# Kernel tuning notes

Hardware: AMD Instinct MI355X
Metric: run time of the kernel (lower is better)

The kernel has to match this reference:

```python
import jax, jax.numpy as jnp
import numpy as np

HEADS = 16
DIM_HEAD = 64
DIM = 1024
MLP = 4096
SCALE = DIM_HEAD ** -0.5
EPS = 1e-5


def _layernorm(x, g, b):
    m = jnp.mean(x, axis=-1, keepdims=True)
    v = jnp.var(x, axis=-1, keepdims=True)
    return (x - m) * jax.lax.rsqrt(v + EPS) * g + b


def _attention(q_in, k_in, qw, kw, vw, ow, ob):
    # v = k (per module); weights stored [in, out]
    b = q_in.shape[0]
    def split(t):  # b n (h d) -> b h n d
        return t.reshape(b, t.shape[1], HEADS, DIM_HEAD).transpose(0, 2, 1, 3)
    q = split(q_in @ qw)
    k = split(k_in @ kw)
    v = split(k_in @ vw)
    dots = jnp.einsum('bhid,bhjd->bhij', q, k) * SCALE
    attn = jax.nn.softmax(dots, axis=-1)
    out = jnp.einsum('bhij,bhjd->bhid', attn, v)
    out = out.transpose(0, 2, 1, 3).reshape(b, out.shape[2], HEADS * DIM_HEAD)
    return out @ ow + ob


def setup_inputs() -> dict:
    key = jax.random.key(0)
    ks = jax.random.split(key, 24)
    def w(k, shape, fan_in):
        return jax.random.normal(k, shape, jnp.float32) * (fan_in ** -0.5)
    inner = HEADS * DIM_HEAD
    return {
        'x': jax.random.normal(ks[0], (4, 4096, DIM), jnp.float32),
        'p': jax.random.normal(ks[1], (4, 256, DIM), jnp.float32),
        'pq_w': w(ks[2], (DIM, inner), DIM), 'pk_w': w(ks[3], (DIM, inner), DIM),
        'pv_w': w(ks[4], (DIM, inner), DIM),
        'po_w': w(ks[5], (inner, DIM), inner), 'po_b': jnp.zeros((DIM,), jnp.float32),
        'xq_w': w(ks[6], (DIM, inner), DIM), 'xk_w': w(ks[7], (DIM, inner), DIM),
        'xv_w': w(ks[8], (DIM, inner), DIM),
        'xo_w': w(ks[9], (inner, DIM), inner), 'xo_b': jnp.zeros((DIM,), jnp.float32),
        'pn_g': jnp.ones((DIM,), jnp.float32), 'pn_b': jnp.zeros((DIM,), jnp.float32),
        'xn_g': jnp.ones((DIM,), jnp.float32), 'xn_b': jnp.zeros((DIM,), jnp.float32),
        'w1': w(ks[10], (DIM, MLP), DIM), 'b1': jnp.zeros((MLP,), jnp.float32),
        'w2': w(ks[11], (MLP, DIM), MLP), 'b2': jnp.zeros((DIM,), jnp.float32),
        'fn_g': jnp.ones((DIM,), jnp.float32), 'fn_b': jnp.zeros((DIM,), jnp.float32),
    }


def reference(x, p, pq_w, pk_w, pv_w, po_w, po_b, xq_w, xk_w, xv_w, xo_w, xo_b,
              pn_g, pn_b, xn_g, xn_b, w1, b1, w2, b2, fn_g, fn_b):
    # p attends to x
    p_att = _attention(p, x, pq_w, pk_w, pv_w, po_w, po_b)
    p_new = _layernorm(p_att + p, pn_g, pn_b)
    # x attends to p_att (note: keys/values come from p_att, not p_new)
    x_att = _attention(x, p_att, xq_w, xk_w, xv_w, xo_w, xo_b)
    x = _layernorm(x_att + x, xn_g, xn_b)
    x_ff = jax.nn.gelu(x @ w1 + b1, approximate=False) @ w2 + b2
    x = _layernorm(x_ff + x, fn_g, fn_b)
    return (x, p_new)
```

## Files before the change

kernel.cpp:

```cpp
#include <hip/hip_runtime.h>


typedef short bf16x8 __attribute__((ext_vector_type(8)));
typedef float f32x4 __attribute__((ext_vector_type(4)));
typedef unsigned int u32x2 __attribute__((ext_vector_type(2)));
typedef unsigned int u32x4v __attribute__((ext_vector_type(4)));

__device__ __forceinline__ unsigned cvt_pk_bf16(float a, float b) {
  unsigned r;
  asm("v_cvt_pk_bf16_f32 %0, %1, %2" : "=v"(r) : "v"(a), "v"(b));
  return r;
}
__device__ __forceinline__ bf16x8 mk8(u32x2 a, u32x2 b) {
  u32x4v t; t.x = a.x; t.y = a.y; t.z = b.x; t.w = b.y;
  return __builtin_bit_cast(bf16x8, t);
}

#define AST 36
#define SEL_LO 0x05040100u
#define SEL_HI 0x07060302u

__global__ __launch_bounds__(256, 2) void gemm_kernel(
    const float* __restrict__ A, int lda,
    const float* __restrict__ Bw, int ldb,
    const float* __restrict__ bias,
    float* __restrict__ C, int ldc,
    int K, int flags)
{
  __shared__ __align__(16) unsigned short Ah[128 * AST];
  __shared__ __align__(16) unsigned short Al[128 * AST];
  __shared__ __align__(16) unsigned short Bh[128 * AST];
  __shared__ __align__(16) unsigned short Bl[128 * AST];

  const int tid = threadIdx.x;
  const int bid   = blockIdx.y * gridDim.x + blockIdx.x;
  const int chunk = (gridDim.x * gridDim.y) >> 3;
  const int lg    = (bid & 7) * chunk + (bid >> 3);
  const int bcol  = (lg % gridDim.x) * 128;
  const int brow  = (lg / gridDim.x) * 128;

  const int lane = tid & 63;
  const int w    = tid >> 6;
  const int wr   = (w >> 1) * 64;
  const int wc   = (w & 1) * 64;
  const int ti   = lane & 15;
  const int g    = lane >> 4;

  const int arow = tid >> 3;
  const int ac4  = (tid & 7) * 4;
  const int K0   = (tid >> 5) * 4;
  const int n4   = (tid & 31) * 4;
  int bwa[4];
#pragma unroll
  for (int i = 0; i < 4; i++)
    bwa[i] = (n4 + i) * AST + ((K0 + 4 * (((n4 + i) >> 2) & 7)) & 31);
  int brofs[4], brbase[4];
#pragma unroll
  for (int nb = 0; nb < 4; nb++) {
    int n = wc + nb * 16 + ti;
    brbase[nb] = n * AST;
    brofs[nb]  = (4 * g + 4 * ((n >> 2) & 7)) & 31;
  }

  f32x4 acc[4][4];
#pragma unroll
  for (int m = 0; m < 4; m++)
#pragma unroll
    for (int n = 0; n < 4; n++) acc[m][n] = (f32x4){0.f, 0.f, 0.f, 0.f};

  float4 fA[4], fB[4];
#pragma unroll
  for (int q = 0; q < 4; q++) {
    fA[q] = *(const float4*)(A + (size_t)(brow + arow + 32 * q) * lda + ac4);
    fB[q] = *(const float4*)(Bw + (size_t)(K0 + q) * ldb + bcol + n4);
  }

  for (int kb = 0; kb < K; kb += 32) {
    __syncthreads();
#pragma unroll
    for (int q = 0; q < 4; q++) {
      float4 f = fA[q];
      unsigned h01 = cvt_pk_bf16(f.x, f.y);
      unsigned h23 = cvt_pk_bf16(f.z, f.w);
      unsigned l01 = cvt_pk_bf16(f.x - __uint_as_float(h01 << 16),
                                 f.y - __uint_as_float(h01 & 0xffff0000u));
      unsigned l23 = cvt_pk_bf16(f.z - __uint_as_float(h23 << 16),
                                 f.w - __uint_as_float(h23 & 0xffff0000u));
      int el = (arow + 32 * q) * AST + ac4;
      *(uint2*)&Ah[el] = make_uint2(h01, h23);
      *(uint2*)&Al[el] = make_uint2(l01, l23);
    }
    {
      unsigned h01[4], h23[4], l01[4], l23[4];
#pragma unroll
      for (int q = 0; q < 4; q++) {
        float4 f = fB[q];
        h01[q] = cvt_pk_bf16(f.x, f.y);
        h23[q] = cvt_pk_bf16(f.z, f.w);
        l01[q] = cvt_pk_bf16(f.x - __uint_as_float(h01[q] << 16),
                             f.y - __uint_as_float(h01[q] & 0xffff0000u));
        l23[q] = cvt_pk_bf16(f.z - __uint_as_float(h23[q] << 16),
                             f.w - __uint_as_float(h23[q] & 0xffff0000u));
      }
      uint2 vh[4], vl[4];
      vh[0] = make_uint2(__builtin_amdgcn_perm(h01[1], h01[0], SEL_LO),
                         __builtin_amdgcn_perm(h01[3], h01[2], SEL_LO));
      vh[1] = make_uint2(__builtin_amdgcn_perm(h01[1], h01[0], SEL_HI),
                         __builtin_amdgcn_perm(h01[3], h01[2], SEL_HI));
      vh[2] = make_uint2(__builtin_amdgcn_perm(h23[1], h23[0], SEL_LO),
                         __builtin_amdgcn_perm(h23[3], h23[2], SEL_LO));
      vh[3] = make_uint2(__builtin_amdgcn_perm(h23[1], h23[0], SEL_HI),
                         __builtin_amdgcn_perm(h23[3], h23[2], SEL_HI));
      vl[0] = make_uint2(__builtin_amdgcn_perm(l01[1], l01[0], SEL_LO),
                         __builtin_amdgcn_perm(l01[3], l01[2], SEL_LO));
      vl[1] = make_uint2(__builtin_amdgcn_perm(l01[1], l01[0], SEL_HI),
                         __builtin_amdgcn_perm(l01[3], l01[2], SEL_HI));
      vl[2] = make_uint2(__builtin_amdgcn_perm(l23[1], l23[0], SEL_LO),
                         __builtin_amdgcn_perm(l23[3], l23[2], SEL_LO));
      vl[3] = make_uint2(__builtin_amdgcn_perm(l23[1], l23[0], SEL_HI),
                         __builtin_amdgcn_perm(l23[3], l23[2], SEL_HI));
#pragma unroll
      for (int i = 0; i < 4; i++) {
        *(uint2*)&Bh[bwa[i]] = vh[i];
        *(uint2*)&Bl[bwa[i]] = vl[i];
      }
    }
    __syncthreads();

    if (kb + 32 < K) {
#pragma unroll
      for (int q = 0; q < 4; q++) {
        fA[q] = *(const float4*)(A + (size_t)(brow + arow + 32 * q) * lda + kb + 32 + ac4);
        fB[q] = *(const float4*)(Bw + (size_t)(kb + 32 + K0 + q) * ldb + bcol + n4);
      }
    }

    u32x2 fa_h[4][2], fa_l[4][2], fb_h[4][2], fb_l[4][2];
#pragma unroll
    for (int m = 0; m < 4; m++) {
      int e0 = (wr + m * 16 + ti) * AST + 4 * g;
      fa_h[m][0] = *(const u32x2*)&Ah[e0];
      fa_h[m][1] = *(const u32x2*)&Ah[e0 + 16];
      fa_l[m][0] = *(const u32x2*)&Al[e0];
      fa_l[m][1] = *(const u32x2*)&Al[e0 + 16];
    }
#pragma unroll
    for (int nb = 0; nb < 4; nb++) {
      int e0 = brbase[nb] + brofs[nb];
      int e1 = brbase[nb] + (brofs[nb] ^ 16);
      fb_h[nb][0] = *(const u32x2*)&Bh[e0];
      fb_h[nb][1] = *(const u32x2*)&Bh[e1];
      fb_l[nb][0] = *(const u32x2*)&Bl[e0];
      fb_l[nb][1] = *(const u32x2*)&Bl[e1];
    }

#pragma unroll
    for (int m = 0; m < 4; m++) {
      bf16x8 ah = mk8(fa_h[m][0], fa_h[m][1]);
      bf16x8 al = mk8(fa_l[m][0], fa_l[m][1]);
#pragma unroll
      for (int n = 0; n < 4; n++) {
        bf16x8 bh = mk8(fb_h[n][0], fb_h[n][1]);
        bf16x8 bl = mk8(fb_l[n][0], fb_l[n][1]);
        acc[m][n] = __builtin_amdgcn_mfma_f32_16x16x32_bf16(ah, bh, acc[m][n], 0, 0, 0);
        acc[m][n] = __builtin_amdgcn_mfma_f32_16x16x32_bf16(al, bh, acc[m][n], 0, 0, 0);
        acc[m][n] = __builtin_amdgcn_mfma_f32_16x16x32_bf16(ah, bl, acc[m][n], 0, 0, 0);
      }
    }
  }

  const int rg = g * 4;
#pragma unroll
  for (int n = 0; n < 4; n++) {
    int col = bcol + wc + n * 16 + ti;
    float bv = (flags & 1) ? bias[col] : 0.0f;
#pragma unroll
    for (int m = 0; m < 4; m++) {
#pragma unroll
      for (int j = 0; j < 4; j++) {
        int row = brow + wr + m * 16 + rg + j;
        float v = acc[m][n][j] + bv;
        if (flags & 2) v = 0.5f * v * (1.0f + erff(v * 0.70710678118654752f));
        size_t off = (size_t)row * ldc + col;
        if (flags & 4) v += C[off];
        C[off] = v;
      }
    }
  }
}

__device__ __forceinline__ int ASW(int row, int k) {
  return row * 64 + ((((k >> 2) ^ (row >> 2)) & 15) * 4) + (k & 3);
}

__global__ __launch_bounds__(256) void attn_kernel(
    const float* __restrict__ Q, const float* __restrict__ K,
    const float* __restrict__ V, float* __restrict__ O,
    int Nq, int Nk)
{
  __shared__ __align__(16) float Qs[64 * 64];
  __shared__ __align__(16) float Ks[64 * 64];
  __shared__ __align__(16) float Vs[64 * 64];

  const int tid = threadIdx.x;
  const int nqt = Nq >> 6;
  const int qt  = blockIdx.x % nqt;
  const int h   = (blockIdx.x / nqt) & 15;
  const int b   = blockIdx.x / (nqt * 16);

  const float* Qb = Q + ((size_t)b * Nq + qt * 64) * 1024 + h * 64;
  const float* Kb = K + (size_t)b * Nk * 1024 + h * 64;
  const float* Vb = V + (size_t)b * Nk * 1024 + h * 64;

#pragma unroll
  for (int q = 0; q < 4; q++) {
    int s = tid + q * 256;
    int i = s >> 4, d4 = (s & 15) * 4;
    float4 f = *(const float4*)(Qb + (size_t)i * 1024 + d4);
    f.x *= 0.125f; f.y *= 0.125f; f.z *= 0.125f; f.w *= 0.125f;
    *(float4*)&Qs[ASW(i, d4)] = f;
  }

  const int ti = tid >> 4, tj = tid & 15;
  const int i0 = ti * 4, j0 = tj * 4;
  float m_r[4] = {-1e30f, -1e30f, -1e30f, -1e30f};
  float l_r[4] = {0.f, 0.f, 0.f, 0.f};
  float o[4][4] = {};

  for (int kt = 0; kt < Nk; kt += 64) {
    __syncthreads();
#pragma unroll
    for (int q = 0; q < 4; q++) {
      int s = tid + q * 256;
      int j = s >> 4, d4 = (s & 15) * 4;
      float4 f = *(const float4*)(Kb + (size_t)(kt + j) * 1024 + d4);
      *(float4*)&Ks[ASW(j, d4)] = f;
      float4 gv = *(const float4*)(Vb + (size_t)(kt + j) * 1024 + d4);
      *(float4*)&Vs[ASW(j, d4)] = gv;
    }
    __syncthreads();

    float s4[4][4] = {};
    for (int k = 0; k < 64; k += 4) {
      float4 qv[4], kv[4];
#pragma unroll
      for (int r = 0; r < 4; r++) qv[r] = *(const float4*)&Qs[ASW(i0 + r, k)];
#pragma unroll
      for (int c = 0; c < 4; c++) kv[c] = *(const float4*)&Ks[ASW(j0 + c, k)];
#pragma unroll
      for (int r = 0; r < 4; r++)
#pragma unroll
        for (int c = 0; c < 4; c++)
          s4[r][c] += qv[r].x * kv[c].x + qv[r].y * kv[c].y +
                      qv[r].z * kv[c].z + qv[r].w * kv[c].w;
    }

    float alpha[4], p[4][4];
#pragma unroll
    for (int r = 0; r < 4; r++) {
      float mx = fmaxf(fmaxf(s4[r][0], s4[r][1]), fmaxf(s4[r][2], s4[r][3]));
      mx = fmaxf(mx, __shfl_xor(mx, 1));
      mx = fmaxf(mx, __shfl_xor(mx, 2));
      mx = fmaxf(mx, __shfl_xor(mx, 4));
      mx = fmaxf(mx, __shfl_xor(mx, 8));
      float mn = fmaxf(m_r[r], mx);
      float rs = 0.f;
#pragma unroll
      for (int c = 0; c < 4; c++) { p[r][c] = __expf(s4[r][c] - mn); rs += p[r][c]; }
      rs += __shfl_xor(rs, 1);
      rs += __shfl_xor(rs, 2);
      rs += __shfl_xor(rs, 4);
      rs += __shfl_xor(rs, 8);
      alpha[r] = __expf(m_r[r] - mn);
      l_r[r] = l_r[r] * alpha[r] + rs;
      m_r[r] = mn;
    }

    __syncthreads();
#pragma unroll
    for (int r = 0; r < 4; r++) {
      float4 t = make_float4(p[r][0], p[r][1], p[r][2], p[r][3]);
      *(float4*)&Ks[ASW(i0 + r, j0)] = t;
    }
    __syncthreads();

#pragma unroll
    for (int r = 0; r < 4; r++)
#pragma unroll
      for (int d = 0; d < 4; d++) o[r][d] *= alpha[r];

    for (int j = 0; j < 64; j += 4) {
      float4 pv[4], vv[4];
#pragma unroll
      for (int r = 0; r < 4; r++) pv[r] = *(const float4*)&Ks[ASW(i0 + r, j)];
#pragma unroll
      for (int c = 0; c < 4; c++) vv[c] = *(const float4*)&Vs[ASW(j + c, j0)];
#pragma unroll
      for (int r = 0; r < 4; r++) {
        o[r][0] += pv[r].x * vv[0].x + pv[r].y * vv[1].x + pv[r].z * vv[2].x + pv[r].w * vv[3].x;
        o[r][1] += pv[r].x * vv[0].y + pv[r].y * vv[1].y + pv[r].z * vv[2].y + pv[r].w * vv[3].y;
        o[r][2] += pv[r].x * vv[0].z + pv[r].y * vv[1].z + pv[r].z * vv[2].z + pv[r].w * vv[3].z;
        o[r][3] += pv[r].x * vv[0].w + pv[r].y * vv[1].w + pv[r].z * vv[2].w + pv[r].w * vv[3].w;
      }
    }
  }

#pragma unroll
  for (int r = 0; r < 4; r++) {
    float inv = 1.0f / l_r[r];
    float4 t = make_float4(o[r][0] * inv, o[r][1] * inv, o[r][2] * inv, o[r][3] * inv);
    *(float4*)(O + ((size_t)b * Nq + qt * 64 + i0 + r) * 1024 + h * 64 + j0) = t;
  }
}

__global__ __launch_bounds__(256) void add_ln_kernel(
    const float* __restrict__ A, const float* __restrict__ R,
    const float* __restrict__ g, const float* __restrict__ be,
    float* __restrict__ out)
{
  const int row = blockIdx.x;
  const size_t base = (size_t)row * 1024 + threadIdx.x * 4;
  float4 a = *(const float4*)(A + base);
  float4 r = *(const float4*)(R + base);
  float v0 = a.x + r.x, v1 = a.y + r.y, v2 = a.z + r.z, v3 = a.w + r.w;
  float s  = v0 + v1 + v2 + v3;
  float ss = v0 * v0 + v1 * v1 + v2 * v2 + v3 * v3;
#pragma unroll
  for (int m = 1; m < 64; m <<= 1) { s += __shfl_xor(s, m); ss += __shfl_xor(ss, m); }
  __shared__ float red[8];
  const int wid = threadIdx.x >> 6;
  if ((threadIdx.x & 63) == 0) { red[wid] = s; red[4 + wid] = ss; }
  __syncthreads();
  s  = red[0] + red[1] + red[2] + red[3];
  ss = red[4] + red[5] + red[6] + red[7];
  float mean = s * (1.0f / 1024.0f);
  float var  = ss * (1.0f / 1024.0f) - mean * mean;
  float inv  = 1.0f / sqrtf(var + 1e-5f);
  float4 gg = *(const float4*)(g + threadIdx.x * 4);
  float4 bb = *(const float4*)(be + threadIdx.x * 4);
  float4 ov;
  ov.x = (v0 - mean) * inv * gg.x + bb.x;
  ov.y = (v1 - mean) * inv * gg.y + bb.y;
  ov.z = (v2 - mean) * inv * gg.z + bb.z;
  ov.w = (v3 - mean) * inv * gg.w + bb.w;
  *(float4*)(out + base) = ov;
}

extern "C" void kernel_launch(void* const* d_in, const int* in_sizes, int n_in,
                              void* d_out, int out_size, void* d_ws, size_t ws_size,
                              hipStream_t stream)
{
  const float* x    = (const float*)d_in[0];
  const float* p    = (const float*)d_in[1];
  const float* pq_w = (const float*)d_in[2];
  const float* pk_w = (const float*)d_in[3];
  const float* pv_w = (const float*)d_in[4];
  const float* po_w = (const float*)d_in[5];
  const float* po_b = (const float*)d_in[6];
  const float* xq_w = (const float*)d_in[7];
  const float* xk_w = (const float*)d_in[8];
  const float* xv_w = (const float*)d_in[9];
  const float* xo_w = (const float*)d_in[10];
  const float* xo_b = (const float*)d_in[11];
  const float* pn_g = (const float*)d_in[12];
  const float* pn_b = (const float*)d_in[13];
  const float* xn_g = (const float*)d_in[14];
  const float* xn_b = (const float*)d_in[15];
  const float* w1   = (const float*)d_in[16];
  const float* b1   = (const float*)d_in[17];
  const float* w2   = (const float*)d_in[18];
  const float* b2   = (const float*)d_in[19];
  const float* fn_g = (const float*)d_in[20];
  const float* fn_b = (const float*)d_in[21];

  float* out_x = (float*)d_out;
  float* out_p = out_x + 16777216;

  float* ws = (float*)d_ws;
  float* W0 = ws;
  float* W1 = ws + 16777216;
  float* S0 = ws + 33554432;
  float* S1 = S0 + 1048576;
  float* S2 = S1 + 1048576;
  float* S3 = S2 + 1048576;

  const dim3 blk(256, 1, 1);
#define GEMM(A_, lda_, B_, ldb_, bias_, C_, ldc_, M_, N_, K_, fl_)              \
  gemm_kernel<<<dim3((N_) / 128, (M_) / 128, 1), blk, 0, stream>>>(             \
      A_, lda_, B_, ldb_, bias_, C_, ldc_, K_, fl_)

  GEMM(p, 1024, pq_w, 1024, nullptr, S0, 1024, 1024, 1024, 1024, 0);
  GEMM(x, 1024, pk_w, 1024, nullptr, W0, 1024, 16384, 1024, 1024, 0);
  GEMM(x, 1024, pv_w, 1024, nullptr, W1, 1024, 16384, 1024, 1024, 0);
  attn_kernel<<<dim3(4 * 16 * (256 / 64)), blk, 0, stream>>>(S0, W0, W1, S1, 256, 4096);
  GEMM(S1, 1024, po_w, 1024, po_b, S2, 1024, 1024, 1024, 1024, 1);
  add_ln_kernel<<<dim3(1024), blk, 0, stream>>>(S2, p, pn_g, pn_b, out_p);

  GEMM(x, 1024, xq_w, 1024, nullptr, W0, 1024, 16384, 1024, 1024, 0);
  GEMM(S2, 1024, xk_w, 1024, nullptr, S0, 1024, 1024, 1024, 1024, 0);
  GEMM(S2, 1024, xv_w, 1024, nullptr, S3, 1024, 1024, 1024, 1024, 0);
  attn_kernel<<<dim3(4 * 16 * (4096 / 64)), blk, 0, stream>>>(W0, S0, S3, W1, 4096, 256);
  GEMM(W1, 1024, xo_w, 1024, xo_b, W0, 1024, 16384, 1024, 1024, 1);
  add_ln_kernel<<<dim3(16384), blk, 0, stream>>>(W0, x, xn_g, xn_b, out_x);

  for (int nt = 0; nt < 4; nt++) {
    GEMM(out_x, 1024, w1 + nt * 1024, 4096, b1 + nt * 1024, W0, 1024,
         16384, 1024, 1024, 1 | 2);
    GEMM(W0, 1024, w2 + (size_t)nt * 1024 * 1024, 1024,
         (nt == 0) ? b2 : nullptr, W1, 1024, 16384, 1024, 1024,
         (nt == 0) ? 1 : 4);
  }
  add_ln_kernel<<<dim3(16384), blk, 0, stream>>>(W1, out_x, fn_g, fn_b, out_x);
#undef GEMM
}
```

Baseline: 2.856 ms.

## Move attention kernel onto bf16 MFMA with split-precision QK and rotated LDS layout

Rewrites the attention kernel to use 16x16x32 bf16 MFMA instead of scalar fp32 FMAs. QK^T uses a hi/lo bf16 split (three MFMAs) to keep near-fp32 accuracy, while P·V uses a single bf16 MFMA with V transposed into LDS. Each wave now owns 16 query rows, so the P tile is written to wave-private LDS rows and the extra block barriers are gone. The cost is lower precision in P and V, plus extra conversion and permute work during tile loads.

```diff
diff --git a/kernel.cpp b/kernel.cpp
--- a/kernel.cpp
+++ b/kernel.cpp
@@ -189,18 +189,16 @@
   }
 }
 
-__device__ __forceinline__ int ASW(int row, int k) {
-  return row * 64 + ((((k >> 2) ^ (row >> 2)) & 15) * 4) + (k & 3);
-}
-
 __global__ __launch_bounds__(256) void attn_kernel(
     const float* __restrict__ Q, const float* __restrict__ K,
     const float* __restrict__ V, float* __restrict__ O,
     int Nq, int Nk)
 {
-  __shared__ __align__(16) float Qs[64 * 64];
-  __shared__ __align__(16) float Ks[64 * 64];
-  __shared__ __align__(16) float Vs[64 * 64];
+  __shared__ __align__(16) unsigned short Qh[64 * 72];
+  __shared__ __align__(16) unsigned short Ql[64 * 72];
+  __shared__ __align__(16) unsigned short Kh[64 * 72];
+  __shared__ __align__(16) unsigned short Kl[64 * 72];
+  __shared__ __align__(16) unsigned short Vh[64 * 72];
 
   const int tid = threadIdx.x;
   const int nqt = Nq >> 6;
@@ -212,105 +210,166 @@
   const float* Kb = K + (size_t)b * Nk * 1024 + h * 64;
   const float* Vb = V + (size_t)b * Nk * 1024 + h * 64;
 
-#pragma unroll
-  for (int q = 0; q < 4; q++) {
-    int s = tid + q * 256;
-    int i = s >> 4, d4 = (s & 15) * 4;
-    float4 f = *(const float4*)(Qb + (size_t)i * 1024 + d4);
+  const int lane  = tid & 63;
+  const int w     = tid >> 6;
+  const int ti    = lane & 15;
+  const int g     = lane >> 4;
+  const int rot16 = 4 * (ti & 7);
+
+  const int krow = tid >> 2;
+  const int kd   = (tid & 3) * 16;
+  const int krot = 4 * (krow & 7);
+  const int vkq  = (tid >> 4) * 4;
+  const int vd4  = (tid & 15) * 4;
+  const int vcol = (vkq + 4 * ((tid & 15) & 7)) & 63;
+  int rotv[4];
+#pragma unroll
+  for (int df = 0; df < 4; df++) rotv[df] = 4 * ((4 * df + (ti >> 2)) & 7);
+
+#pragma unroll
+  for (int i = 0; i < 4; i++) {
+    float4 f = *(const float4*)(Qb + (size_t)krow * 1024 + kd + 4 * i);
     f.x *= 0.125f; f.y *= 0.125f; f.z *= 0.125f; f.w *= 0.125f;
-    *(float4*)&Qs[ASW(i, d4)] = f;
-  }
-
-  const int ti = tid >> 4, tj = tid & 15;
-  const int i0 = ti * 4, j0 = tj * 4;
+    unsigned h01 = cvt_pk_bf16(f.x, f.y);
+    unsigned h23 = cvt_pk_bf16(f.z, f.w);
+    unsigned l01 = cvt_pk_bf16(f.x - __uint_as_float(h01 << 16),
+                               f.y - __uint_as_float(h01 & 0xffff0000u));
+    unsigned l23 = cvt_pk_bf16(f.z - __uint_as_float(h23 << 16),
+                               f.w - __uint_as_float(h23 & 0xffff0000u));
+    int el = krow * 72 + ((kd + 4 * i + krot) & 63);
+    *(uint2*)&Qh[el] = make_uint2(h01, h23);
+    *(uint2*)&Ql[el] = make_uint2(l01, l23);
+  }
+  __syncthreads();
+
+  bf16x8 qh8[2], ql8[2];
+  {
+    int qrb = (16 * w + ti) * 72;
+#pragma unroll
+    for (int kc = 0; kc < 2; kc++) {
+      int c0 = (kc * 32 + 4 * g + rot16) & 63;
+      int c1 = (kc * 32 + 4 * g + 16 + rot16) & 63;
+      qh8[kc] = mk8(*(const u32x2*)&Qh[qrb + c0], *(const u32x2*)&Qh[qrb + c1]);
+      ql8[kc] = mk8(*(const u32x2*)&Ql[qrb + c0], *(const u32x2*)&Ql[qrb + c1]);
+    }
+  }
+
+  f32x4 acc_o[4];
+#pragma unroll
+  for (int df = 0; df < 4; df++) acc_o[df] = (f32x4){0.f, 0.f, 0.f, 0.f};
   float m_r[4] = {-1e30f, -1e30f, -1e30f, -1e30f};
   float l_r[4] = {0.f, 0.f, 0.f, 0.f};
-  float o[4][4] = {};
 
   for (int kt = 0; kt < Nk; kt += 64) {
     __syncthreads();
 #pragma unroll
-    for (int q = 0; q < 4; q++) {
-      int s = tid + q * 256;
-      int j = s >> 4, d4 = (s & 15) * 4;
-      float4 f = *(const float4*)(Kb + (size_t)(kt + j) * 1024 + d4);
-      *(float4*)&Ks[ASW(j, d4)] = f;
-      float4 gv = *(const float4*)(Vb + (size_t)(kt + j) * 1024 + d4);
-      *(float4*)&Vs[ASW(j, d4)] = gv;
+    for (int i = 0; i < 4; i++) {
+      float4 f = *(const float4*)(Kb + (size_t)(kt + krow) * 1024 + kd + 4 * i);
+      unsigned h01 = cvt_pk_bf16(f.x, f.y);
+      unsigned h23 = cvt_pk_bf16(f.z, f.w);
+      unsigned l01 = cvt_pk_bf16(f.x - __uint_as_float(h01 << 16),
+                                 f.y - __uint_as_float(h01 & 0xffff0000u));
+      unsigned l23 = cvt_pk_bf16(f.z - __uint_as_float(h23 << 16),
+                                 f.w - __uint_as_float(h23 & 0xffff0000u));
+      int el = krow * 72 + ((kd + 4 * i + krot) & 63);
+      *(uint2*)&Kh[el] = make_uint2(h01, h23);
+      *(uint2*)&Kl[el] = make_uint2(l01, l23);
+    }
+    {
+      unsigned h01[4], h23[4];
+#pragma unroll
+      for (int q = 0; q < 4; q++) {
+        float4 f = *(const float4*)(Vb + (size_t)(kt + vkq + q) * 1024 + vd4);
+        h01[q] = cvt_pk_bf16(f.x, f.y);
+        h23[q] = cvt_pk_bf16(f.z, f.w);
+      }
+      uint2 t0 = make_uint2(__builtin_amdgcn_perm(h01[1], h01[0], SEL_LO),
+                            __builtin_amdgcn_perm(h01[3], h01[2], SEL_LO));
+      uint2 t1 = make_uint2(__builtin_amdgcn_perm(h01[1], h01[0], SEL_HI),
+                            __builtin_amdgcn_perm(h01[3], h01[2], SEL_HI));
+      uint2 t2 = make_uint2(__builtin_amdgcn_perm(h23[1], h23[0], SEL_LO),
+                            __builtin_amdgcn_perm(h23[3], h23[2], SEL_LO));
+      uint2 t3 = make_uint2(__builtin_amdgcn_perm(h23[1], h23[0], SEL_HI),
+                            __builtin_amdgcn_perm(h23[3], h23[2], SEL_HI));
+      *(uint2*)&Vh[(vd4 + 0) * 72 + vcol] = t0;
+      *(uint2*)&Vh[(vd4 + 1) * 72 + vcol] = t1;
+      *(uint2*)&Vh[(vd4 + 2) * 72 + vcol] = t2;
+      *(uint2*)&Vh[(vd4 + 3) * 72 + vcol] = t3;
     }
     __syncthreads();
 
-    float s4[4][4] = {};
-    for (int k = 0; k < 64; k += 4) {
-      float4 qv[4], kv[4];
-#pragma unroll
-      for (int r = 0; r < 4; r++) qv[r] = *(const float4*)&Qs[ASW(i0 + r, k)];
-#pragma unroll
-      for (int c = 0; c < 4; c++) kv[c] = *(const float4*)&Ks[ASW(j0 + c, k)];
-#pragma unroll
-      for (int r = 0; r < 4; r++)
-#pragma unroll
-        for (int c = 0; c < 4; c++)
-          s4[r][c] += qv[r].x * kv[c].x + qv[r].y * kv[c].y +
-                      qv[r].z * kv[c].z + qv[r].w * kv[c].w;
-    }
-
-    float alpha[4], p[4][4];
-#pragma unroll
-    for (int r = 0; r < 4; r++) {
-      float mx = fmaxf(fmaxf(s4[r][0], s4[r][1]), fmaxf(s4[r][2], s4[r][3]));
+    f32x4 sc[4];
+#pragma unroll
+    for (int nf = 0; nf < 4; nf++) sc[nf] = (f32x4){0.f, 0.f, 0.f, 0.f};
+#pragma unroll
+    for (int nf = 0; nf < 4; nf++) {
+      int rb = (16 * nf + ti) * 72;
+#pragma unroll
+      for (int kc = 0; kc < 2; kc++) {
+        int c0 = (kc * 32 + 4 * g + rot16) & 63;
+        int c1 = (kc * 32 + 4 * g + 16 + rot16) & 63;
+        bf16x8 bh = mk8(*(const u32x2*)&Kh[rb + c0], *(const u32x2*)&Kh[rb + c1]);
+        bf16x8 bl = mk8(*(const u32x2*)&Kl[rb + c0], *(const u32x2*)&Kl[rb + c1]);
+        sc[nf] = __builtin_amdgcn_mfma_f32_16x16x32_bf16(qh8[kc], bh, sc[nf], 0, 0, 0);
+        sc[nf] = __builtin_amdgcn_mfma_f32_16x16x32_bf16(ql8[kc], bh, sc[nf], 0, 0, 0);
+        sc[nf] = __builtin_amdgcn_mfma_f32_16x16x32_bf16(qh8[kc], bl, sc[nf], 0, 0, 0);
+      }
+    }
+
+    float pr[4][4];
+#pragma unroll
+    for (int j = 0; j < 4; j++) {
+      float mx = fmaxf(fmaxf(sc[0][j], sc[1][j]), fmaxf(sc[2][j], sc[3][j]));
       mx = fmaxf(mx, __shfl_xor(mx, 1));
       mx = fmaxf(mx, __shfl_xor(mx, 2));
       mx = fmaxf(mx, __shfl_xor(mx, 4));
       mx = fmaxf(mx, __shfl_xor(mx, 8));
-      float mn = fmaxf(m_r[r], mx);
+      float mn = fmaxf(m_r[j], mx);
+      float al = __expf(m_r[j] - mn);
       float rs = 0.f;
 #pragma unroll
-      for (int c = 0; c < 4; c++) { p[r][c] = __expf(s4[r][c] - mn); rs += p[r][c]; }
+      for (int nf = 0; nf < 4; nf++) { pr[nf][j] = __expf(sc[nf][j] - mn); rs += pr[nf][j]; }
       rs += __shfl_xor(rs, 1);
       rs += __shfl_xor(rs, 2);
       rs += __shfl_xor(rs, 4);
       rs += __shfl_xor(rs, 8);
-      alpha[r] = __expf(m_r[r] - mn);
-      l_r[r] = l_r[r] * alpha[r] + rs;
-      m_r[r] = mn;
-    }
-
-    __syncthreads();
-#pragma unroll
-    for (int r = 0; r < 4; r++) {
-      float4 t = make_float4(p[r][0], p[r][1], p[r][2], p[r][3]);
-      *(float4*)&Ks[ASW(i0 + r, j0)] = t;
-    }
-    __syncthreads();
-
-#pragma unroll
-    for (int r = 0; r < 4; r++)
-#pragma unroll
-      for (int d = 0; d < 4; d++) o[r][d] *= alpha[r];
-
-    for (int j = 0; j < 64; j += 4) {
-      float4 pv[4], vv[4];
-#pragma unroll
-      for (int r = 0; r < 4; r++) pv[r] = *(const float4*)&Ks[ASW(i0 + r, j)];
-#pragma unroll
-      for (int c = 0; c < 4; c++) vv[c] = *(const float4*)&Vs[ASW(j + c, j0)];
-#pragma unroll
-      for (int r = 0; r < 4; r++) {
-        o[r][0] += pv[r].x * vv[0].x + pv[r].y * vv[1].x + pv[r].z * vv[2].x + pv[r].w * vv[3].x;
-        o[r][1] += pv[r].x * vv[0].y + pv[r].y * vv[1].y + pv[r].z * vv[2].y + pv[r].w * vv[3].y;
-        o[r][2] += pv[r].x * vv[0].z + pv[r].y * vv[1].z + pv[r].z * vv[2].z + pv[r].w * vv[3].z;
-        o[r][3] += pv[r].x * vv[0].w + pv[r].y * vv[1].w + pv[r].z * vv[2].w + pv[r].w * vv[3].w;
-      }
-    }
-  }
-
-#pragma unroll
-  for (int r = 0; r < 4; r++) {
-    float inv = 1.0f / l_r[r];
-    float4 t = make_float4(o[r][0] * inv, o[r][1] * inv, o[r][2] * inv, o[r][3] * inv);
-    *(float4*)(O + ((size_t)b * Nq + qt * 64 + i0 + r) * 1024 + h * 64 + j0) = t;
-  }
+      l_r[j] = l_r[j] * al + rs;
+      m_r[j] = mn;
+#pragma unroll
+      for (int df = 0; df < 4; df++) acc_o[df][j] *= al;
+    }
+
+#pragma unroll
+    for (int nf = 0; nf < 4; nf++)
+#pragma unroll
+      for (int j = 0; j < 4; j++)
+        Qh[(16 * w + 4 * g + j) * 72 + 16 * nf + ti] =
+            (unsigned short)cvt_pk_bf16(pr[nf][j], pr[nf][j]);
+
+#pragma unroll
+    for (int kc = 0; kc < 2; kc++) {
+      int ab = (16 * w + ti) * 72 + kc * 32 + 4 * g;
+      bf16x8 pa = mk8(*(const u32x2*)&Qh[ab], *(const u32x2*)&Qh[ab + 16]);
+#pragma unroll
+      for (int df = 0; df < 4; df++) {
+        int rb = (16 * df + ti) * 72;
+        int c0 = (kc * 32 + 4 * g + rotv[df]) & 63;
+        int c1 = (kc * 32 + 4 * g + 16 + rotv[df]) & 63;
+        bf16x8 vb = mk8(*(const u32x2*)&Vh[rb + c0], *(const u32x2*)&Vh[rb + c1]);
+        acc_o[df] = __builtin_amdgcn_mfma_f32_16x16x32_bf16(pa, vb, acc_o[df], 0, 0, 0);
+      }
+    }
+  }
+
+  float inv[4];
+#pragma unroll
+  for (int j = 0; j < 4; j++) inv[j] = 1.0f / l_r[j];
+#pragma unroll
+  for (int df = 0; df < 4; df++)
+#pragma unroll
+    for (int j = 0; j < 4; j++)
+      O[((size_t)b * Nq + qt * 64 + 16 * w + 4 * g + j) * 1024 + h * 64 + 16 * df + ti] =
+          acc_o[df][j] * inv[j];
 }
 
 __global__ __launch_bounds__(256) void add_ln_kernel(
```

New measurement: 2.287 ms. 1.25x faster.
